# Kernel tuning notes

Measured on AMD Instinct MI355X. Metric: run time of the kernel, lower is better.

Reference implementation:

```python
import jax, jax.numpy as jnp
import numpy as np

B, C, H, W = 4, 256, 64, 64
CI = C // 2
EPS = 1e-5


def setup_inputs() -> dict:
    key = jax.random.key(0)
    ks = jax.random.split(key, 3)
    return {
        "x": jax.random.normal(ks[0], (B, C, H, W), dtype=jnp.float32) * 0.1,
        "g_w": jax.random.normal(ks[1], (CI, C), dtype=jnp.float32) * 0.05,
        "g_b": jnp.zeros((CI,), dtype=jnp.float32),
        "W_w": jax.random.normal(ks[2], (C, CI), dtype=jnp.float32) * 0.05,
        "W_b": jnp.zeros((C,), dtype=jnp.float32),
        "gamma": jnp.ones((C,), dtype=jnp.float32),
        "beta": jnp.zeros((C,), dtype=jnp.float32),
    }


def reference(x, g_w, g_b, W_w, W_b, gamma, beta):
    b, c, h, w = x.shape
    n = h * w
    ci = g_w.shape[0]
    # g: 1x1 conv C -> C/2
    g_x = jnp.einsum('oc,bchw->bohw', g_w, x) + g_b[None, :, None, None]
    g_x = g_x.reshape(b, ci, n).transpose(0, 2, 1)          # [B, N, Ci]
    theta = x.reshape(b, c, n).transpose(0, 2, 1)           # [B, N, C]
    phi = x.reshape(b, c, n)                                # [B, C, N]
    f = jnp.einsum('bnc,bcm->bnm', theta, phi)              # [B, N, N]
    attn = jax.nn.softmax(f, axis=-1)
    y = jnp.einsum('bnm,bmc->bnc', attn, g_x)               # [B, N, Ci]
    y = y.transpose(0, 2, 1).reshape(b, ci, h, w)
    # W: 1x1 conv C/2 -> C, then BatchNorm2d (training-mode batch stats)
    wy = jnp.einsum('oc,bchw->bohw', W_w, y) + W_b[None, :, None, None]
    mean = wy.mean(axis=(0, 2, 3))
    var = wy.var(axis=(0, 2, 3))  # biased, as torch BN uses for normalization
    wy = (wy - mean[None, :, None, None]) * jax.lax.rsqrt(var[None, :, None, None] + EPS)
    wy = wy * gamma[None, :, None, None] + beta[None, :, None, None]
    return wy + x
```

## Files before the change

kernel.cpp:

```cpp
#include <hip/hip_runtime.h>
#include <math.h>

#define B_ 4
#define C_ 256
#define CI_ 128
#define N_ 4096
#define QT_ 128
#define KT_ 64
#define KH_ 2048
#define NITER (KH_ / KT_)
#define KSTRIDE 264
#define VSTRIDE 72
#define WSTR 66
#define YSTR 68
constexpr float EPS_ = 1e-5f;

typedef __attribute__((ext_vector_type(8))) short bfrag;
typedef __attribute__((ext_vector_type(4))) float f4;

__device__ __forceinline__ unsigned short bf16r(float x) {
    unsigned u = __float_as_uint(x);
    u += 0x7FFFu + ((u >> 16) & 1u);
    return (unsigned short)(u >> 16);
}
__device__ __forceinline__ unsigned pack_bf16(float a, float b) {
    unsigned ua = __float_as_uint(a); ua += 0x7FFFu + ((ua >> 16) & 1u);
    unsigned ub = __float_as_uint(b); ub += 0x7FFFu + ((ub >> 16) & 1u);
    return (ua >> 16) | (ub & 0xFFFF0000u);
}

__global__ void zero_acc(float* __restrict__ sums) {
    int t = threadIdx.x;
    sums[t] = 0.f;
    sums[t + 256] = 0.f;
}

__global__ __launch_bounds__(256) void make_xt(const float* __restrict__ x,
                                               unsigned short* __restrict__ xt) {
    int n  = blockIdx.x * 256 + threadIdx.x;
    int c0 = blockIdx.y * 8;
    int b  = blockIdx.z;
    const float* xb = x + (size_t)b * C_ * N_;
    unsigned short buf[8];
#pragma unroll
    for (int c = 0; c < 8; c++) buf[c] = bf16r(xb[(c0 + c) * N_ + n]);
    uint4 v;
    v.x = buf[0] | ((unsigned)buf[1] << 16);
    v.y = buf[2] | ((unsigned)buf[3] << 16);
    v.z = buf[4] | ((unsigned)buf[5] << 16);
    v.w = buf[6] | ((unsigned)buf[7] << 16);
    *(uint4*)&xt[((size_t)b * N_ + n) * C_ + c0] = v;
}

__global__ __launch_bounds__(256) void gconv(const float* __restrict__ x,
                                             const float* __restrict__ gw,
                                             const float* __restrict__ gb,
                                             unsigned short* __restrict__ gx) {
    int m  = blockIdx.x * 256 + threadIdx.x;
    int o0 = blockIdx.y * 16;
    int b  = blockIdx.z;
    const float* xb = x + (size_t)b * C_ * N_;
    float acc[16];
#pragma unroll
    for (int o = 0; o < 16; o++) acc[o] = gb[o0 + o];
    for (int c = 0; c < C_; c++) {
        float xv = xb[c * N_ + m];
#pragma unroll
        for (int o = 0; o < 16; o++) acc[o] += gw[(o0 + o) * C_ + c] * xv;
    }
#pragma unroll
    for (int o = 0; o < 16; o++)
        gx[((size_t)b * CI_ + o0 + o) * N_ + m] = bf16r(acc[o]);
}

__global__ __launch_bounds__(512, 1) void attn(const unsigned short* __restrict__ xt,
                                               const unsigned short* __restrict__ gx,
                                               float* __restrict__ Yp,
                                               float* __restrict__ ml) {
    __shared__ __align__(16) unsigned short Ks[2][64 * KSTRIDE];
    __shared__ __align__(16) unsigned short Vs[2][128 * VSTRIDE];
    __shared__ __align__(16) unsigned short Ps[128 * VSTRIDE];

    const int tid  = threadIdx.x;
    const int lane = tid & 63, w = tid >> 6;
    const int quad = lane >> 4, ql = lane & 15;
    const int half = blockIdx.x & 1;
    const int b    = (blockIdx.x & 7) >> 1;
    const int qt   = blockIdx.x >> 3;
    const int n0   = qt * QT_;
    const int kbase = half * KH_;
    const unsigned short* xtb = xt + (size_t)b * N_ * C_;
    const unsigned short* gxb = gx + (size_t)b * CI_ * N_;

    bfrag qb[8];
#pragma unroll
    for (int ks = 0; ks < 8; ks++)
        qb[ks] = *(const bfrag*)(xtb + (size_t)(n0 + 16 * w + ql) * C_ + 32 * ks + quad * 8);

    f4 yacc[8];
    const f4 zero4 = {0.f, 0.f, 0.f, 0.f};
#pragma unroll
    for (int i = 0; i < 8; i++) yacc[i] = zero4;
    float mrun = -INFINITY, lrun = 0.f;

    uint4 kreg[4], vreg[2];
#pragma unroll
    for (int r = 0; r < 4; r++) {
        int idx = r * 512 + tid;
        kreg[r] = *(const uint4*)(xtb + (size_t)(kbase + (idx >> 5)) * C_ + (idx & 31) * 8);
    }
#pragma unroll
    for (int r = 0; r < 2; r++) {
        int idx = r * 512 + tid;
        vreg[r] = *(const uint4*)(gxb + (size_t)(idx >> 3) * N_ + kbase + (idx & 7) * 8);
    }
#pragma unroll
    for (int r = 0; r < 4; r++) {
        int idx = r * 512 + tid;
        *(uint4*)&Ks[0][(idx >> 5) * KSTRIDE + (idx & 31) * 8] = kreg[r];
    }
#pragma unroll
    for (int r = 0; r < 2; r++) {
        int idx = r * 512 + tid;
        *(uint4*)&Vs[0][(idx >> 3) * VSTRIDE + (idx & 7) * 8] = vreg[r];
    }
#pragma unroll
    for (int r = 0; r < 4; r++) {
        int idx = r * 512 + tid;
        kreg[r] = *(const uint4*)(xtb + (size_t)(kbase + KT_ + (idx >> 5)) * C_ + (idx & 31) * 8);
    }
#pragma unroll
    for (int r = 0; r < 2; r++) {
        int idx = r * 512 + tid;
        vreg[r] = *(const uint4*)(gxb + (size_t)(idx >> 3) * N_ + kbase + KT_ + (idx & 7) * 8);
    }
    __syncthreads();

    for (int it = 0; it < NITER; ++it) {
        const int cur = it & 1, nxt = cur ^ 1;

        if (it + 1 < NITER) {
#pragma unroll
            for (int r = 0; r < 4; r++) {
                int idx = r * 512 + tid;
                *(uint4*)&Ks[nxt][(idx >> 5) * KSTRIDE + (idx & 31) * 8] = kreg[r];
            }
#pragma unroll
            for (int r = 0; r < 2; r++) {
                int idx = r * 512 + tid;
                *(uint4*)&Vs[nxt][(idx >> 3) * VSTRIDE + (idx & 7) * 8] = vreg[r];
            }
        }
        if (it + 2 < NITER) {
            const int t0 = kbase + (it + 2) * KT_;
#pragma unroll
            for (int r = 0; r < 4; r++) {
                int idx = r * 512 + tid;
                kreg[r] = *(const uint4*)(xtb + (size_t)(t0 + (idx >> 5)) * C_ + (idx & 31) * 8);
            }
#pragma unroll
            for (int r = 0; r < 2; r++) {
                int idx = r * 512 + tid;
                vreg[r] = *(const uint4*)(gxb + (size_t)(idx >> 3) * N_ + t0 + (idx & 7) * 8);
            }
        }

        f4 sacc[4];
#pragma unroll
        for (int i = 0; i < 4; i++) sacc[i] = zero4;
#pragma unroll
        for (int ks = 0; ks < 8; ks++) {
            bfrag ka[4];
#pragma unroll
            for (int i = 0; i < 4; i++)
                ka[i] = *(const bfrag*)&Ks[cur][(16 * i + ql) * KSTRIDE + 32 * ks + quad * 8];
#pragma unroll
            for (int i = 0; i < 4; i++)
                sacc[i] = __builtin_amdgcn_mfma_f32_16x16x32_bf16(ka[i], qb[ks], sacc[i], 0, 0, 0);
        }

        float mx = -INFINITY;
#pragma unroll
        for (int i = 0; i < 4; i++)
#pragma unroll
            for (int r = 0; r < 4; r++) mx = fmaxf(mx, sacc[i][r]);
        mx = fmaxf(mx, __shfl_xor(mx, 16, 64));
        mx = fmaxf(mx, __shfl_xor(mx, 32, 64));
        float mn = fmaxf(mrun, mx);
        float alpha = __expf(mrun - mn);
        mrun = mn;
        lrun *= alpha;
        if (__any(alpha != 1.f)) {
#pragma unroll
            for (int i = 0; i < 8; i++) {
                yacc[i][0] *= alpha; yacc[i][1] *= alpha;
                yacc[i][2] *= alpha; yacc[i][3] *= alpha;
            }
        }

        {
            int q = 16 * w + ql;
            float lsum = 0.f;
#pragma unroll
            for (int i = 0; i < 4; i++) {
                float p0 = __expf(sacc[i][0] - mrun);
                float p1 = __expf(sacc[i][1] - mrun);
                float p2 = __expf(sacc[i][2] - mrun);
                float p3 = __expf(sacc[i][3] - mrun);
                lsum += (p0 + p1) + (p2 + p3);
                int idx = q * VSTRIDE + 16 * i + 4 * quad;
                *(unsigned*)&Ps[idx]     = pack_bf16(p0, p1);
                *(unsigned*)&Ps[idx + 2] = pack_bf16(p2, p3);
            }
            lrun += lsum;
        }

#pragma unroll
        for (int ks = 0; ks < 2; ks++) {
            bfrag pb, va[8];
            pb = *(const bfrag*)&Ps[(16 * w + ql) * VSTRIDE + 32 * ks + quad * 8];
#pragma unroll
            for (int i = 0; i < 8; i++)
                va[i] = *(const bfrag*)&Vs[cur][(16 * i + ql) * VSTRIDE + 32 * ks + quad * 8];
#pragma unroll
            for (int i = 0; i < 8; i++)
                yacc[i] = __builtin_amdgcn_mfma_f32_16x16x32_bf16(va[i], pb, yacc[i], 0, 0, 0);
        }

        __syncthreads();
    }

    lrun += __shfl_xor(lrun, 16, 64);
    lrun += __shfl_xor(lrun, 32, 64);
    {
        int n = n0 + 16 * w + ql;
#pragma unroll
        for (int i = 0; i < 8; i++)
#pragma unroll
            for (int r = 0; r < 4; r++) {
                int ci = 16 * i + quad * 4 + r;
                Yp[(((size_t)half * 4 + b) * CI_ + ci) * N_ + n] = yacc[i][r];
            }
        if (quad == 0) {
            ml[(((size_t)half * 4 + b) * N_ + n) * 2]     = mrun;
            ml[(((size_t)half * 4 + b) * N_ + n) * 2 + 1] = lrun;
        }
    }
}

__global__ __launch_bounds__(256, 2) void merge_wconv(const float* __restrict__ Yp,
                                                      const float* __restrict__ ml,
                                                      const float* __restrict__ Ww,
                                                      const float* __restrict__ Wb,
                                                      float* __restrict__ wy,
                                                      float* __restrict__ sums) {
    __shared__ float Ws[128 * WSTR];
    __shared__ float Ys[128 * YSTR];
    __shared__ float wqs[2][64];

    const int tid = threadIdx.x;
    const int nl = tid & 63, cig = tid >> 6;
    const int lane = tid & 63, w = tid >> 6;
    const int ng = lane & 15, cg = lane >> 4;
    const int n0 = blockIdx.x * 64, b = blockIdx.y, z = blockIdx.z;

#pragma unroll
    for (int r = 0; r < 8; r++) {
        int idx = r * 256 + tid;
        int cop = idx >> 5;
        int k4  = idx & 31;
        float4 f = *(const float4*)&Ww[(size_t)(64 * z + cop) * CI_ + 4 * k4];
        Ws[(4 * k4 + 0) * WSTR + cop] = f.x;
        Ws[(4 * k4 + 1) * WSTR + cop] = f.y;
        Ws[(4 * k4 + 2) * WSTR + cop] = f.z;
        Ws[(4 * k4 + 3) * WSTR + cop] = f.w;
    }

    if (tid < 64) {
        float m0 = ml[((size_t)b * N_ + n0 + tid) * 2];
        float l0 = ml[((size_t)b * N_ + n0 + tid) * 2 + 1];
        float m1 = ml[(((size_t)4 + b) * N_ + n0 + tid) * 2];
        float l1 = ml[(((size_t)4 + b) * N_ + n0 + tid) * 2 + 1];
        float mm = fmaxf(m0, m1);
        float e0 = __expf(m0 - mm), e1 = __expf(m1 - mm);
        float inv = 1.f / (e0 * l0 + e1 * l1);
        wqs[0][tid] = e0 * inv;
        wqs[1][tid] = e1 * inv;
    }
    __syncthreads();

    float w0 = wqs[0][nl], w1 = wqs[1][nl];
#pragma unroll
    for (int j = 0; j < 32; j++) {
        int ci = cig * 32 + j;
        size_t base = ((size_t)b * CI_ + ci) * N_ + n0 + nl;
        Ys[ci * YSTR + nl] = w0 * Yp[base] + w1 * Yp[(size_t)4 * CI_ * N_ + base];
    }
    __syncthreads();

    const int cop0 = 16 * w + 4 * cg;
    float acc[4][4];
#pragma unroll
    for (int j = 0; j < 4; j++) {
        float bias = Wb[64 * z + cop0 + j];
#pragma unroll
        for (int d = 0; d < 4; d++) acc[j][d] = bias;
    }
#pragma unroll 4
    for (int k = 0; k < CI_; k++) {
        float4 yv = *(const float4*)&Ys[k * YSTR + 4 * ng];
        float4 wv = *(const float4*)&Ws[k * WSTR + cop0];
        acc[0][0] += wv.x * yv.x; acc[0][1] += wv.x * yv.y;
        acc[0][2] += wv.x * yv.z; acc[0][3] += wv.x * yv.w;
        acc[1][0] += wv.y * yv.x; acc[1][1] += wv.y * yv.y;
        acc[1][2] += wv.y * yv.z; acc[1][3] += wv.y * yv.w;
        acc[2][0] += wv.z * yv.x; acc[2][1] += wv.z * yv.y;
        acc[2][2] += wv.z * yv.z; acc[2][3] += wv.z * yv.w;
        acc[3][0] += wv.w * yv.x; acc[3][1] += wv.w * yv.y;
        acc[3][2] += wv.w * yv.z; acc[3][3] += wv.w * yv.w;
    }

#pragma unroll
    for (int j = 0; j < 4; j++) {
        int co = 64 * z + cop0 + j;
        float4 st;
        st.x = acc[j][0]; st.y = acc[j][1]; st.z = acc[j][2]; st.w = acc[j][3];
        *(float4*)&wy[((size_t)b * C_ + co) * N_ + n0 + 4 * ng] = st;

        float s1 = acc[j][0] + acc[j][1] + acc[j][2] + acc[j][3];
        float s2 = acc[j][0] * acc[j][0] + acc[j][1] * acc[j][1]
                 + acc[j][2] * acc[j][2] + acc[j][3] * acc[j][3];
#pragma unroll
        for (int off = 1; off < 16; off <<= 1) {
            s1 += __shfl_xor(s1, off, 64);
            s2 += __shfl_xor(s2, off, 64);
        }
        if (ng == 0) {
            atomicAdd(&sums[co], s1);
            atomicAdd(&sums[256 + co], s2);
        }
    }
}

__global__ __launch_bounds__(256) void bn_finalize(float* __restrict__ wy,
                                                   const float* __restrict__ x,
                                                   const float* __restrict__ sums,
                                                   const float* __restrict__ gamma,
                                                   const float* __restrict__ beta,
                                                   float* __restrict__ out) {
    int n4 = blockIdx.x * 256 + threadIdx.x;
    int co = blockIdx.y;
    int b  = blockIdx.z;
    float cnt  = (float)(B_ * N_);
    float mean = sums[co] / cnt;
    float var  = sums[256 + co] / cnt - mean * mean;
    float sc   = rsqrtf(var + EPS_) * gamma[co];
    float bt   = beta[co];
    size_t idx = ((size_t)b * C_ + co) * N_ + (size_t)n4 * 4;
    float4 wv = *(const float4*)&wy[idx];
    float4 xv = *(const float4*)&x[idx];
    float4 o;
    o.x = (wv.x - mean) * sc + bt + xv.x;
    o.y = (wv.y - mean) * sc + bt + xv.y;
    o.z = (wv.z - mean) * sc + bt + xv.z;
    o.w = (wv.w - mean) * sc + bt + xv.w;
    *(float4*)&out[idx] = o;
}

extern "C" void kernel_launch(void* const* d_in, const int* in_sizes, int n_in,
                              void* d_out, int out_size, void* d_ws, size_t ws_size,
                              hipStream_t stream) {
    const float* x     = (const float*)d_in[0];
    const float* gw    = (const float*)d_in[1];
    const float* gb    = (const float*)d_in[2];
    const float* Ww    = (const float*)d_in[3];
    const float* Wb    = (const float*)d_in[4];
    const float* gamma = (const float*)d_in[5];
    const float* beta  = (const float*)d_in[6];
    float* out = (float*)d_out;
    float* ws  = (float*)d_ws;

    unsigned short* xt  = (unsigned short*)ws;
    unsigned short* gxb = (unsigned short*)(ws + 2097152);
    float* Yp   = ws + 3145728;
    float* ml   = ws + 7340032;
    float* sums = ws + 7405568;
    float* wy   = out;

    hipLaunchKernelGGL(zero_acc, dim3(1), dim3(256), 0, stream, sums);
    hipLaunchKernelGGL(make_xt, dim3(16, 32, 4), dim3(256), 0, stream, x, xt);
    hipLaunchKernelGGL(gconv, dim3(16, 8, 4), dim3(256), 0, stream, x, gw, gb, gxb);
    hipLaunchKernelGGL(attn, dim3(256), dim3(512), 0, stream, xt, gxb, Yp, ml);
    hipLaunchKernelGGL(merge_wconv, dim3(64, 4, 4), dim3(256), 0, stream, Yp, ml, Ww, Wb, wy, sums);
    hipLaunchKernelGGL(bn_finalize, dim3(4, 256, 4), dim3(256), 0, stream, wy, x, sums, gamma, beta, out);
}
```

Before: 299.4 us.

## Split merge_wconv into merge and wconv_stats, fold zeroing into make_xt, widen P stores

The fused merge+W-conv kernel, which staged data in shared memory, is replaced by two kernels. One is a vectorized merge that writes y into the workspace. The other is a register-blocked 1x1 conv that reads W weights straight from global memory and reduces the BN statistics per block before issuing atomics. The zero_acc launch is folded into make_xt, and the attention P writes are merged into one 64-bit LDS store. This saves a launch and cuts the number of atomics, but it adds a round trip of y through global memory and leaves the W reads uncached in LDS.

```diff
diff --git a/kernel.cpp b/kernel.cpp
--- a/kernel.cpp
+++ b/kernel.cpp
@@ -11,8 +11,6 @@
 #define NITER (KH_ / KT_)
 #define KSTRIDE 264
 #define VSTRIDE 72
-#define WSTR 66
-#define YSTR 68
 constexpr float EPS_ = 1e-5f;
 
 typedef __attribute__((ext_vector_type(8))) short bfrag;
@@ -29,14 +27,13 @@
     return (ua >> 16) | (ub & 0xFFFF0000u);
 }
 
-__global__ void zero_acc(float* __restrict__ sums) {
-    int t = threadIdx.x;
-    sums[t] = 0.f;
-    sums[t + 256] = 0.f;
-}
-
 __global__ __launch_bounds__(256) void make_xt(const float* __restrict__ x,
-                                               unsigned short* __restrict__ xt) {
+                                               unsigned short* __restrict__ xt,
+                                               float* __restrict__ sums) {
+    if (blockIdx.x == 0 && blockIdx.y == 0 && blockIdx.z == 0) {
+        sums[threadIdx.x] = 0.f;
+        sums[threadIdx.x + 256] = 0.f;
+    }
     int n  = blockIdx.x * 256 + threadIdx.x;
     int c0 = blockIdx.y * 8;
     int b  = blockIdx.z;
@@ -209,8 +206,9 @@
                 float p3 = __expf(sacc[i][3] - mrun);
                 lsum += (p0 + p1) + (p2 + p3);
                 int idx = q * VSTRIDE + 16 * i + 4 * quad;
-                *(unsigned*)&Ps[idx]     = pack_bf16(p0, p1);
-                *(unsigned*)&Ps[idx + 2] = pack_bf16(p2, p3);
+                unsigned long long pv = (unsigned long long)pack_bf16(p0, p1)
+                                      | ((unsigned long long)pack_bf16(p2, p3) << 32);
+                *(unsigned long long*)&Ps[idx] = pv;
             }
             lrun += lsum;
         }
@@ -248,97 +246,81 @@
     }
 }
 
-__global__ __launch_bounds__(256, 2) void merge_wconv(const float* __restrict__ Yp,
-                                                      const float* __restrict__ ml,
-                                                      const float* __restrict__ Ww,
-                                                      const float* __restrict__ Wb,
-                                                      float* __restrict__ wy,
-                                                      float* __restrict__ sums) {
-    __shared__ float Ws[128 * WSTR];
-    __shared__ float Ys[128 * YSTR];
-    __shared__ float wqs[2][64];
-
-    const int tid = threadIdx.x;
-    const int nl = tid & 63, cig = tid >> 6;
-    const int lane = tid & 63, w = tid >> 6;
-    const int ng = lane & 15, cg = lane >> 4;
-    const int n0 = blockIdx.x * 64, b = blockIdx.y, z = blockIdx.z;
-
-#pragma unroll
-    for (int r = 0; r < 8; r++) {
-        int idx = r * 256 + tid;
-        int cop = idx >> 5;
-        int k4  = idx & 31;
-        float4 f = *(const float4*)&Ww[(size_t)(64 * z + cop) * CI_ + 4 * k4];
-        Ws[(4 * k4 + 0) * WSTR + cop] = f.x;
-        Ws[(4 * k4 + 1) * WSTR + cop] = f.y;
-        Ws[(4 * k4 + 2) * WSTR + cop] = f.z;
-        Ws[(4 * k4 + 3) * WSTR + cop] = f.w;
-    }
-
-    if (tid < 64) {
-        float m0 = ml[((size_t)b * N_ + n0 + tid) * 2];
-        float l0 = ml[((size_t)b * N_ + n0 + tid) * 2 + 1];
-        float m1 = ml[(((size_t)4 + b) * N_ + n0 + tid) * 2];
-        float l1 = ml[(((size_t)4 + b) * N_ + n0 + tid) * 2 + 1];
-        float mm = fmaxf(m0, m1);
-        float e0 = __expf(m0 - mm), e1 = __expf(m1 - mm);
-        float inv = 1.f / (e0 * l0 + e1 * l1);
-        wqs[0][tid] = e0 * inv;
-        wqs[1][tid] = e1 * inv;
+__global__ __launch_bounds__(256) void merge(const float* __restrict__ Yp,
+                                             const float* __restrict__ ml,
+                                             float* __restrict__ y) {
+    int n4 = blockIdx.x * 256 + threadIdx.x;
+    int ci = blockIdx.y;
+    int b  = blockIdx.z;
+    int n  = n4 * 4;
+    float4 a0 = *(const float4*)&ml[((size_t)b * N_ + n) * 2];
+    float4 a1 = *(const float4*)&ml[((size_t)b * N_ + n + 2) * 2];
+    float4 c0 = *(const float4*)&ml[(((size_t)4 + b) * N_ + n) * 2];
+    float4 c1 = *(const float4*)&ml[(((size_t)4 + b) * N_ + n + 2) * 2];
+    float m0[4] = {a0.x, a0.z, a1.x, a1.z};
+    float l0[4] = {a0.y, a0.w, a1.y, a1.w};
+    float m1[4] = {c0.x, c0.z, c1.x, c1.z};
+    float l1[4] = {c0.y, c0.w, c1.y, c1.w};
+    float w0[4], w1[4];
+#pragma unroll
+    for (int k = 0; k < 4; k++) {
+        float mm = fmaxf(m0[k], m1[k]);
+        float e0 = __expf(m0[k] - mm), e1 = __expf(m1[k] - mm);
+        float inv = 1.f / (e0 * l0[k] + e1 * l1[k]);
+        w0[k] = e0 * inv;
+        w1[k] = e1 * inv;
+    }
+    size_t base = ((size_t)b * CI_ + ci) * N_ + n;
+    float4 y0 = *(const float4*)&Yp[base];
+    float4 y1 = *(const float4*)&Yp[(size_t)4 * CI_ * N_ + base];
+    float4 o;
+    o.x = w0[0] * y0.x + w1[0] * y1.x;
+    o.y = w0[1] * y0.y + w1[1] * y1.y;
+    o.z = w0[2] * y0.z + w1[2] * y1.z;
+    o.w = w0[3] * y0.w + w1[3] * y1.w;
+    *(float4*)&y[base] = o;
+}
+
+__global__ __launch_bounds__(256) void wconv_stats(const float* __restrict__ y,
+                                                   const float* __restrict__ Ww,
+                                                   const float* __restrict__ Wb,
+                                                   float* __restrict__ wy,
+                                                   float* __restrict__ sums) {
+    int n   = blockIdx.x * 256 + threadIdx.x;
+    int co0 = blockIdx.y * 16;
+    int b   = blockIdx.z;
+    const float* yb = y + (size_t)b * CI_ * N_;
+    float acc[16];
+#pragma unroll
+    for (int o = 0; o < 16; o++) acc[o] = Wb[co0 + o];
+    for (int ci = 0; ci < CI_; ci++) {
+        float yv = yb[ci * N_ + n];
+#pragma unroll
+        for (int o = 0; o < 16; o++) acc[o] += Ww[(co0 + o) * CI_ + ci] * yv;
+    }
+    float* wyb = wy + (size_t)b * C_ * N_;
+#pragma unroll
+    for (int o = 0; o < 16; o++) wyb[(co0 + o) * N_ + n] = acc[o];
+
+    __shared__ float wred[32][4];
+    int lane = threadIdx.x & 63, wid = threadIdx.x >> 6;
+#pragma unroll
+    for (int o = 0; o < 16; o++) {
+        float s1 = acc[o], s2 = acc[o] * acc[o];
+#pragma unroll
+        for (int off = 32; off > 0; off >>= 1) {
+            s1 += __shfl_down(s1, off, 64);
+            s2 += __shfl_down(s2, off, 64);
+        }
+        if (lane == 0) { wred[o][wid] = s1; wred[16 + o][wid] = s2; }
     }
     __syncthreads();
-
-    float w0 = wqs[0][nl], w1 = wqs[1][nl];
-#pragma unroll
-    for (int j = 0; j < 32; j++) {
-        int ci = cig * 32 + j;
-        size_t base = ((size_t)b * CI_ + ci) * N_ + n0 + nl;
-        Ys[ci * YSTR + nl] = w0 * Yp[base] + w1 * Yp[(size_t)4 * CI_ * N_ + base];
-    }
-    __syncthreads();
-
-    const int cop0 = 16 * w + 4 * cg;
-    float acc[4][4];
-#pragma unroll
-    for (int j = 0; j < 4; j++) {
-        float bias = Wb[64 * z + cop0 + j];
-#pragma unroll
-        for (int d = 0; d < 4; d++) acc[j][d] = bias;
-    }
-#pragma unroll 4
-    for (int k = 0; k < CI_; k++) {
-        float4 yv = *(const float4*)&Ys[k * YSTR + 4 * ng];
-        float4 wv = *(const float4*)&Ws[k * WSTR + cop0];
-        acc[0][0] += wv.x * yv.x; acc[0][1] += wv.x * yv.y;
-        acc[0][2] += wv.x * yv.z; acc[0][3] += wv.x * yv.w;
-        acc[1][0] += wv.y * yv.x; acc[1][1] += wv.y * yv.y;
-        acc[1][2] += wv.y * yv.z; acc[1][3] += wv.y * yv.w;
-        acc[2][0] += wv.z * yv.x; acc[2][1] += wv.z * yv.y;
-        acc[2][2] += wv.z * yv.z; acc[2][3] += wv.z * yv.w;
-        acc[3][0] += wv.w * yv.x; acc[3][1] += wv.w * yv.y;
-        acc[3][2] += wv.w * yv.z; acc[3][3] += wv.w * yv.w;
-    }
-
-#pragma unroll
-    for (int j = 0; j < 4; j++) {
-        int co = 64 * z + cop0 + j;
-        float4 st;
-        st.x = acc[j][0]; st.y = acc[j][1]; st.z = acc[j][2]; st.w = acc[j][3];
-        *(float4*)&wy[((size_t)b * C_ + co) * N_ + n0 + 4 * ng] = st;
-
-        float s1 = acc[j][0] + acc[j][1] + acc[j][2] + acc[j][3];
-        float s2 = acc[j][0] * acc[j][0] + acc[j][1] * acc[j][1]
-                 + acc[j][2] * acc[j][2] + acc[j][3] * acc[j][3];
-#pragma unroll
-        for (int off = 1; off < 16; off <<= 1) {
-            s1 += __shfl_xor(s1, off, 64);
-            s2 += __shfl_xor(s2, off, 64);
-        }
-        if (ng == 0) {
-            atomicAdd(&sums[co], s1);
-            atomicAdd(&sums[256 + co], s2);
-        }
+    if (threadIdx.x < 32) {
+        int q = threadIdx.x;
+        float t = wred[q][0] + wred[q][1] + wred[q][2] + wred[q][3];
+        int o = q & 15;
+        if (q < 16) atomicAdd(&sums[co0 + o], t);
+        else        atomicAdd(&sums[256 + co0 + o], t);
     }
 }
 
@@ -385,12 +367,13 @@
     float* Yp   = ws + 3145728;
     float* ml   = ws + 7340032;
     float* sums = ws + 7405568;
+    float* y    = ws;
     float* wy   = out;
 
-    hipLaunchKernelGGL(zero_acc, dim3(1), dim3(256), 0, stream, sums);
-    hipLaunchKernelGGL(make_xt, dim3(16, 32, 4), dim3(256), 0, stream, x, xt);
+    hipLaunchKernelGGL(make_xt, dim3(16, 32, 4), dim3(256), 0, stream, x, xt, sums);
     hipLaunchKernelGGL(gconv, dim3(16, 8, 4), dim3(256), 0, stream, x, gw, gb, gxb);
     hipLaunchKernelGGL(attn, dim3(256), dim3(512), 0, stream, xt, gxb, Yp, ml);
-    hipLaunchKernelGGL(merge_wconv, dim3(64, 4, 4), dim3(256), 0, stream, Yp, ml, Ww, Wb, wy, sums);
+    hipLaunchKernelGGL(merge, dim3(4, 128, 4), dim3(256), 0, stream, Yp, ml, y);
+    hipLaunchKernelGGL(wconv_stats, dim3(16, 16, 4), dim3(256), 0, stream, y, Ww, Wb, wy, sums);
     hipLaunchKernelGGL(bn_finalize, dim3(4, 256, 4), dim3(256), 0, stream, wy, x, sums, gamma, beta, out);
 }
```

Measured after the change: 302.5 us. Within noise of the previous version (+1.0%).
